# Performance work log

Hardware: AMD Instinct MI355X
Metric: run time of the kernel (lower is better)

Reference implementation:

```python
import jax, jax.numpy as jnp
import numpy as np

N = 50000      # nodes
E = 800000     # edges
F_IN = 128     # input feature dim (OGBN-MAG paper features)
H = 4          # attention heads
HID = 64       # hidden_dim (per-head out channels)
HC = H * HID   # 256, concat output width
NC = 349       # num_classes
BN_EPS = 1e-5


def setup_inputs() -> dict:
    key = jax.random.key(0)
    ks = jax.random.split(key, 32)
    s = 0.05
    inp = {
        "x": jax.random.normal(ks[0], (N, F_IN), dtype=jnp.float32),
        "edge_index": jax.random.randint(ks[1], (2, E), 0, N, dtype=jnp.int64),
    }
    dins = [F_IN, HC]
    i = 2
    for l in range(2):
        d = dins[l]
        inp[f"ws{l}"] = jax.random.normal(ks[i], (d, HC), jnp.float32) * s; i += 1
        inp[f"wd{l}"] = jax.random.normal(ks[i], (d, HC), jnp.float32) * s; i += 1
        inp[f"atts{l}"] = jax.random.normal(ks[i], (H, HID), jnp.float32) * s; i += 1
        inp[f"attd{l}"] = jax.random.normal(ks[i], (H, HID), jnp.float32) * s; i += 1
        inp[f"bg{l}"] = jnp.zeros((HC,), jnp.float32); i += 1
        inp[f"lw{l}"] = jax.random.normal(ks[i], (d, HC), jnp.float32) * s; i += 1
        inp[f"lb{l}"] = jnp.zeros((HC,), jnp.float32); i += 1
        inp[f"g{l}"] = jnp.ones((HC,), jnp.float32); i += 1
        inp[f"b{l}"] = jnp.zeros((HC,), jnp.float32); i += 1
    inp["fcw"] = jax.random.normal(ks[i], (HC, NC), jnp.float32) * s
    inp["fcb"] = jnp.zeros((NC,), jnp.float32)
    return inp


def _gat(x, src, dst, ws, wd, atts, attd, bias):
    # PyG GATConv: separate src/dst projections, per-edge additive attention,
    # softmax over incoming edges of each dst node, scatter-add aggregation.
    n = x.shape[0]
    xs = (x @ ws).reshape(n, H, HID)            # [N,H,C] source messages
    xd = (x @ wd).reshape(n, H, HID)
    a_s = jnp.einsum("nhc,hc->nh", xs, atts)    # alpha_src
    a_d = jnp.einsum("nhc,hc->nh", xd, attd)    # alpha_dst
    e = jax.nn.leaky_relu(a_s[src] + a_d[dst], 0.2)   # [E,H]
    m = jax.ops.segment_max(e, dst, num_segments=n)   # segment-softmax (stable)
    ex = jnp.exp(e - m[dst])
    den = jax.ops.segment_sum(ex, dst, num_segments=n)
    w = ex / (den[dst] + 1e-16)                 # [E,H]
    out = jax.ops.segment_sum(xs[src] * w[:, :, None], dst, num_segments=n)
    return out.reshape(n, HC) + bias


def _bn(h, gamma, beta):
    # training-mode BatchNorm1d: batch statistics over nodes, biased variance
    mu = jnp.mean(h, axis=0)
    var = jnp.mean(jnp.square(h - mu), axis=0)
    return (h - mu) * jax.lax.rsqrt(var + BN_EPS) * gamma + beta


def reference(x, edge_index, ws0, wd0, atts0, attd0, bg0, lw0, lb0, g0, b0,
              ws1, wd1, atts1, attd1, bg1, lw1, lb1, g1, b1, fcw, fcb):
    src, dst = edge_index[0], edge_index[1]
    h = _gat(x, src, dst, ws0, wd0, atts0, attd0, bg0) + x @ lw0 + lb0
    h = jax.nn.relu(_bn(h, g0, b0))
    h = _gat(h, src, dst, ws1, wd1, atts1, attd1, bg1) + h @ lw1 + lb1
    h = jax.nn.relu(_bn(h, g1, b1))
    return h @ fcw + fcb
```

## Files before the change

kernel.cpp:

```cpp
#include <hip/hip_runtime.h>
#include <hip/hip_bf16.h>
#include <math.h>

#define N_NODES 50000
#define MPAD 50048
#define N_EDGES 800000
#define HCH 256
#define NHEAD 4
#define HIDC 64
#define NCLS 349
#define F_IN 128

typedef short short8 __attribute__((ext_vector_type(8)));
typedef float floatx4 __attribute__((ext_vector_type(4)));

__global__ void k_detect(const unsigned* ei, int* flag) {
    if (blockIdx.x == 0 && threadIdx.x == 0) {
        int i64 = 1;
        for (int e = 0; e < 64; e++)
            if (ei[2 * e + 1] != 0u) { i64 = 0; break; }
        *flag = i64;
    }
}

__device__ __forceinline__ void edge_sd(const int* ei, int e, int i64, int& s, int& d) {
    if (i64) {
        const long long* p = (const long long*)ei;
        s = (int)p[e]; d = (int)p[N_EDGES + e];
    } else {
        s = ei[e]; d = ei[N_EDGES + e];
    }
}

__global__ void k_deg(const int* ei, const int* flag, int* deg) {
    int e = blockIdx.x * 256 + threadIdx.x;
    if (e >= N_EDGES) return;
    int s, d; edge_sd(ei, e, *flag, s, d);
    atomicAdd(&deg[d], 1);
}

__global__ __launch_bounds__(256) void k_scan1(const int* __restrict__ deg,
                                               int* __restrict__ rowptr,
                                               int* __restrict__ bsum) {
    __shared__ int sd[256];
    int t = threadIdx.x;
    int base = blockIdx.x * 1024 + t * 4;
    int d0 = 0, d1 = 0, d2 = 0, d3 = 0;
    if (base + 3 < N_NODES) {
        int4 v = *(const int4*)(deg + base);
        d0 = v.x; d1 = v.y; d2 = v.z; d3 = v.w;
    } else {
        if (base + 0 < N_NODES) d0 = deg[base + 0];
        if (base + 1 < N_NODES) d1 = deg[base + 1];
        if (base + 2 < N_NODES) d2 = deg[base + 2];
        if (base + 3 < N_NODES) d3 = deg[base + 3];
    }
    int ts = d0 + d1 + d2 + d3;
    sd[t] = ts;
    __syncthreads();
    #pragma unroll
    for (int off = 1; off < 256; off <<= 1) {
        int v = (t >= off) ? sd[t - off] : 0;
        __syncthreads();
        sd[t] += v;
        __syncthreads();
    }
    int excl = (t == 0) ? 0 : sd[t - 1];
    if (base + 0 < N_NODES) rowptr[base + 0] = excl;
    if (base + 1 < N_NODES) rowptr[base + 1] = excl + d0;
    if (base + 2 < N_NODES) rowptr[base + 2] = excl + d0 + d1;
    if (base + 3 < N_NODES) rowptr[base + 3] = excl + d0 + d1 + d2;
    if (t == 255) bsum[blockIdx.x] = sd[255];
}

__global__ void k_scan2(int* __restrict__ bsum, int nb, int* __restrict__ rowptr) {
    int lane = threadIdx.x;
    int orig = (lane < nb) ? bsum[lane] : 0;
    int v = orig;
    #pragma unroll
    for (int off = 1; off < 64; off <<= 1) {
        int tv = __shfl_up(v, off, 64);
        if (lane >= off) v += tv;
    }
    if (lane < nb) bsum[lane] = v - orig;
    if (lane == 0) rowptr[N_NODES] = N_EDGES;
}

__global__ __launch_bounds__(256) void k_scan3(int* __restrict__ rowptr,
                                               const int* __restrict__ bsum) {
    int base = blockIdx.x * 1024 + threadIdx.x * 4;
    int off = bsum[blockIdx.x];
    if (base + 3 < N_NODES) {
        int4 v = *(int4*)(rowptr + base);
        v.x += off; v.y += off; v.z += off; v.w += off;
        *(int4*)(rowptr + base) = v;
    } else {
        for (int j = 0; j < 4; j++)
            if (base + j < N_NODES) rowptr[base + j] += off;
    }
}

__global__ void k_fill(const int* ei, const int* flag, const int* __restrict__ rowptr,
                       int* cursor, int* __restrict__ esrc) {
    int e = blockIdx.x * 256 + threadIdx.x;
    if (e >= N_EDGES) return;
    int s, d; edge_sd(ei, e, *flag, s, d);
    int pos = atomicAdd(&cursor[d], 1);
    esrc[rowptr[d] + pos] = s;
}

__global__ void k_wtilde(const float* __restrict__ ws, const float* __restrict__ wd,
                         const float* __restrict__ atts, const float* __restrict__ attd,
                         float* __restrict__ wt, int d) {
    int id = blockIdx.x * 256 + threadIdx.x;
    if (id >= d * 8) return;
    int j = id & 7, k = id >> 3;
    const float* w = (j < 4) ? ws : wd;
    const float* at = (j < 4) ? atts : attd;
    int h = j & 3;
    float s = 0.f;
    for (int c = 0; c < HIDC; c++) s += w[k * HCH + h * HIDC + c] * at[h * HIDC + c];
    wt[k * 8 + j] = s;
}

__device__ __forceinline__ unsigned short b16(float v) {
    __hip_bfloat16 t = __float2bfloat16(v);
    return *(unsigned short*)&t;
}

__device__ __forceinline__ float bfu(unsigned short u) {
    unsigned v = (unsigned)u << 16;
    return __builtin_bit_cast(float, v);
}

__global__ __launch_bounds__(256) void k_xcast(const float* __restrict__ x,
                                               unsigned short* __restrict__ xb) {
    size_t tot = (size_t)N_NODES * 128 / 4;
    for (size_t i = (size_t)blockIdx.x * 256 + threadIdx.x; i < tot;
         i += (size_t)gridDim.x * 256) {
        float4 v = *(const float4*)(x + i * 4);
        ushort4 o = {b16(v.x), b16(v.y), b16(v.z), b16(v.w)};
        *(ushort4*)(xb + i * 4) = o;
    }
}

__global__ void k_wcat_t(const float* __restrict__ ws, const float* __restrict__ lw,
                         const float* __restrict__ wtil, int K,
                         unsigned short* __restrict__ Bb) {
    int id = blockIdx.x * 256 + threadIdx.x;
    if (id >= 640 * K) return;
    int c = id / K, k = id % K;
    float v;
    if (c < 256) v = ws[(size_t)k * 256 + c];
    else if (c < 512) v = lw[(size_t)k * 256 + (c - 256)];
    else if (c < 520) v = wtil[(size_t)k * 8 + (c - 512)];
    else v = 0.f;
    Bb[(size_t)c * K + k] = b16(v);
}

__global__ void k_fcw_t(const float* __restrict__ fcw, int K,
                        unsigned short* __restrict__ Bb) {
    int id = blockIdx.x * 256 + threadIdx.x;
    if (id >= 384 * K) return;
    int c = id / K, k = id % K;
    float v = (c < NCLS) ? fcw[(size_t)k * NCLS + c] : 0.f;
    Bb[(size_t)c * K + k] = b16(v);
}

__device__ __forceinline__ void gload16(const void* g, void* l) {
    __builtin_amdgcn_global_load_lds(
        (const __attribute__((address_space(1))) void*)g,
        (__attribute__((address_space(3))) void*)l, 16, 0, 0);
}

__global__ __launch_bounds__(256) void k_gemm1(
    const unsigned short* __restrict__ Ab,
    const unsigned short* __restrict__ Bb,
    float* __restrict__ C, int ldc, __hip_bfloat16* __restrict__ xsb,
    __hip_bfloat16* __restrict__ linbb, float* __restrict__ aout,
    const float* __restrict__ bias, int M, int K, int Nc) {
    __shared__ unsigned short sA[2][4096];
    __shared__ unsigned short sB[2][4096];
    int tid = threadIdx.x;
    int lane = tid & 63, wave = tid >> 6;
    int wm = wave >> 1, wn = wave & 1;
    int row0 = blockIdx.x * 128, col0 = blockIdx.y * 128;

    int rowq[2], kcq[2];
    #pragma unroll
    for (int q = 0; q < 2; q++) {
        int lds16 = wave * 128 + q * 64 + lane;
        int line = lds16 >> 3;
        int slot0 = (lds16 & 7) ^ (line & 7);
        rowq[q] = (line << 1) | (slot0 >> 2);
        kcq[q] = slot0 & 3;
    }
    int kc = lane >> 4, fr = lane & 15;
    int offA[4], offB[4];
    #pragma unroll
    for (int i = 0; i < 4; i++) {
        int ar = wm * 64 + i * 16 + fr;
        int ln = ar >> 1;
        int sl = (((ar & 1) << 2) | kc) ^ (ln & 7);
        offA[i] = ln * 128 + sl * 16;
        int bc = wn * 64 + i * 16 + fr;
        ln = bc >> 1;
        sl = (((bc & 1) << 2) | kc) ^ (ln & 7);
        offB[i] = ln * 128 + sl * 16;
    }

    const int nt = K >> 5;
    #pragma unroll
    for (int q = 0; q < 2; q++) {
        int lb = wave * 2048 + q * 1024;
        gload16(Ab + (size_t)(row0 + rowq[q]) * K + kcq[q] * 8, (char*)sA[0] + lb);
        gload16(Bb + (size_t)(col0 + rowq[q]) * K + kcq[q] * 8, (char*)sB[0] + lb);
    }

    floatx4 acc[4][4] = {};
    int cur = 0;
    for (int t = 0; t < nt; t++) {
        if (t + 1 < nt) {
            int k0 = (t + 1) << 5;
            #pragma unroll
            for (int q = 0; q < 2; q++) {
                int lb = wave * 2048 + q * 1024;
                gload16(Ab + (size_t)(row0 + rowq[q]) * K + k0 + kcq[q] * 8, (char*)sA[cur ^ 1] + lb);
                gload16(Bb + (size_t)(col0 + rowq[q]) * K + k0 + kcq[q] * 8, (char*)sB[cur ^ 1] + lb);
            }
            asm volatile("s_waitcnt vmcnt(4)" ::: "memory");
        } else {
            asm volatile("s_waitcnt vmcnt(0)" ::: "memory");
        }
        __builtin_amdgcn_s_barrier();
        __builtin_amdgcn_sched_barrier(0);
        short8 fah[4], fbh[4];
        #pragma unroll
        for (int i = 0; i < 4; i++) {
            fah[i] = *(const short8*)((const char*)sA[cur] + offA[i]);
            fbh[i] = *(const short8*)((const char*)sB[cur] + offB[i]);
        }
        #pragma unroll
        for (int i = 0; i < 4; i++)
            #pragma unroll
            for (int j = 0; j < 4; j++)
                acc[i][j] = __builtin_amdgcn_mfma_f32_16x16x32_bf16(fah[i], fbh[j], acc[i][j], 0, 0, 0);
        asm volatile("s_waitcnt lgkmcnt(0)" ::: "memory");
        __builtin_amdgcn_s_barrier();
        __builtin_amdgcn_sched_barrier(0);
        cur ^= 1;
    }
    #pragma unroll
    for (int i = 0; i < 4; i++) {
        #pragma unroll
        for (int j = 0; j < 4; j++) {
            int c = col0 + wn * 64 + j * 16 + fr;
            if (c >= Nc) continue;
            float bv = bias ? bias[c] : 0.f;
            #pragma unroll
            for (int q = 0; q < 4; q++) {
                int r = row0 + wm * 64 + i * 16 + (lane >> 4) * 4 + q;
                if (r >= M) continue;
                float val = acc[i][j][q] + bv;
                if (C) C[(size_t)r * ldc + c] = val;
                else if (c < 256) xsb[(size_t)r * 256 + c] = __float2bfloat16(val);
                else if (c < 512) linbb[(size_t)r * 256 + (c - 256)] = __float2bfloat16(val);
                else aout[(size_t)r * 8 + (c - 512)] = val;
            }
        }
    }
}

#define LEAKY_EXP(vv) __expf(((vv) > 0.f) ? (vv) : 0.2f * (vv))

__global__ __launch_bounds__(256) void k_agg(
    const __hip_bfloat16* __restrict__ xsb,
    const __hip_bfloat16* __restrict__ linb, const float* __restrict__ a,
    const int* __restrict__ rowptr, const int* __restrict__ esrc,
    const float* __restrict__ bg, const float* __restrict__ lb,
    __hip_bfloat16* __restrict__ hout) {
    int wave = threadIdx.x >> 6;
    int lane = threadIdx.x & 63;
    int n = blockIdx.x * 4 + wave;
    if (n >= N_NODES) return;
    int half = lane >> 5;
    int l32 = lane & 31;
    int c0 = l32 * 8;
    int h = l32 >> 3;
    float ad = a[(size_t)n * 8 + 4 + h];
    int beg = rowptr[n], end = rowptr[n + 1];
    float acc[8] = {};
    float dsum = 0.f;
    int k = beg;
    for (; k + 8 <= end; k += 8) {
        int sb = k + half * 4;
        int s[4];
        #pragma unroll
        for (int u = 0; u < 4; u++) s[u] = esrc[sb + u];
        short8 m[4];
        #pragma unroll
        for (int u = 0; u < 4; u++)
            m[u] = *(const short8*)(xsb + (size_t)s[u] * 256 + c0);
        float av[4];
        #pragma unroll
        for (int u = 0; u < 4; u++) av[u] = a[(size_t)s[u] * 8 + h];
        #pragma unroll
        for (int u = 0; u < 4; u++) {
            float ev = LEAKY_EXP(av[u] + ad);
            #pragma unroll
            for (int j = 0; j < 8; j++)
                acc[j] += bfu((unsigned short)m[u][j]) * ev;
            dsum += ev;
        }
    }
    for (; k < end; k += 2) {
        int idx = k + half;
        bool valid = idx < end;
        int s = esrc[valid ? idx : (end - 1)];
        short8 m = *(const short8*)(xsb + (size_t)s * 256 + c0);
        float av = a[(size_t)s * 8 + h];
        float ev = valid ? LEAKY_EXP(av + ad) : 0.f;
        #pragma unroll
        for (int j = 0; j < 8; j++)
            acc[j] += bfu((unsigned short)m[j]) * ev;
        dsum += ev;
    }
    #pragma unroll
    for (int j = 0; j < 8; j++) acc[j] += __shfl_xor(acc[j], 32, 64);
    dsum += __shfl_xor(dsum, 32, 64);
    if (lane < 32) {
        float inv = 1.f / (dsum + 1e-16f);
        float4 bg0 = *(const float4*)(bg + c0);
        float4 bg1 = *(const float4*)(bg + c0 + 4);
        float4 lb0 = *(const float4*)(lb + c0);
        float4 lb1 = *(const float4*)(lb + c0 + 4);
        float bgv[8] = {bg0.x, bg0.y, bg0.z, bg0.w, bg1.x, bg1.y, bg1.z, bg1.w};
        float lbv[8] = {lb0.x, lb0.y, lb0.z, lb0.w, lb1.x, lb1.y, lb1.z, lb1.w};
        short8 lnv = *(const short8*)(linb + (size_t)n * 256 + c0);
        short8 o;
        #pragma unroll
        for (int j = 0; j < 8; j++)
            o[j] = (short)b16(acc[j] * inv + bgv[j] + bfu((unsigned short)lnv[j]) + lbv[j]);
        *(short8*)(hout + (size_t)n * 256 + c0) = o;
    }
}

__global__ void k_bnstats(const __hip_bfloat16* __restrict__ hb,
                          float* __restrict__ bnsum, float* __restrict__ bnsq) {
    int c = threadIdx.x;
    float s = 0.f, q = 0.f;
    for (int r = blockIdx.x; r < N_NODES; r += gridDim.x) {
        float v = __bfloat162float(hb[(size_t)r * 256 + c]);
        s += v; q += v * v;
    }
    atomicAdd(&bnsum[c], s);
    atomicAdd(&bnsq[c], q);
}

__global__ __launch_bounds__(256) void k_bnapply(
    const __hip_bfloat16* __restrict__ hb, __hip_bfloat16* __restrict__ hpost,
    const float* __restrict__ bnsum, const float* __restrict__ bnsq,
    const float* __restrict__ g, const float* __restrict__ b) {
    __shared__ float sA[256], sB[256];
    int t = threadIdx.x;
    {
        float m = bnsum[t] / (float)N_NODES;
        float v = bnsq[t] / (float)N_NODES - m * m;
        float rs = rsqrtf(v + 1e-5f) * g[t];
        sA[t] = rs;
        sB[t] = b[t] - m * rs;
    }
    __syncthreads();
    size_t tot = (size_t)N_NODES * 256;
    for (size_t i = (size_t)blockIdx.x * 256 + t; i < tot;
         i += (size_t)gridDim.x * 256) {
        int c = (int)(i & 255);
        float v = __bfloat162float(hb[i]) * sA[c] + sB[c];
        v = v > 0.f ? v : 0.f;
        hpost[i] = __float2bfloat16(v);
    }
}

extern "C" void kernel_launch(void* const* d_in, const int* in_sizes, int n_in,
                              void* d_out, int out_size, void* d_ws, size_t ws_size,
                              hipStream_t stream) {
    const float* x     = (const float*)d_in[0];
    const int*   ei    = (const int*)d_in[1];
    const float* ws0   = (const float*)d_in[2];
    const float* wd0   = (const float*)d_in[3];
    const float* atts0 = (const float*)d_in[4];
    const float* attd0 = (const float*)d_in[5];
    const float* bg0   = (const float*)d_in[6];
    const float* lw0   = (const float*)d_in[7];
    const float* lb0   = (const float*)d_in[8];
    const float* g0    = (const float*)d_in[9];
    const float* b0    = (const float*)d_in[10];
    const float* ws1   = (const float*)d_in[11];
    const float* wd1   = (const float*)d_in[12];
    const float* atts1 = (const float*)d_in[13];
    const float* attd1 = (const float*)d_in[14];
    const float* bg1   = (const float*)d_in[15];
    const float* lw1   = (const float*)d_in[16];
    const float* lb1   = (const float*)d_in[17];
    const float* g1    = (const float*)d_in[18];
    const float* b1    = (const float*)d_in[19];
    const float* fcw   = (const float*)d_in[20];
    const float* fcb   = (const float*)d_in[21];
    float* out = (float*)d_out;

    char* p = (char*)d_ws;
    auto alloc = [&](size_t bytes) -> char* {
        char* r = p;
        p += (bytes + 255) & ~(size_t)255;
        return r;
    };
    __hip_bfloat16* xsb   = (__hip_bfloat16*)alloc((size_t)N_NODES * 256 * 2);
    __hip_bfloat16* linb  = (__hip_bfloat16*)alloc((size_t)N_NODES * 256 * 2);
    __hip_bfloat16* hb    = (__hip_bfloat16*)alloc((size_t)N_NODES * 256 * 2);
    __hip_bfloat16* hpost = (__hip_bfloat16*)alloc((size_t)MPAD * 256 * 2);
    unsigned short* xb    = (unsigned short*)alloc((size_t)MPAD * 128 * 2);
    float* a      = (float*)alloc((size_t)N_NODES * 8 * 4);
    int*   esrc   = (int*)alloc((size_t)N_EDGES * 4);
    int*   rowptr = (int*)alloc((size_t)(N_NODES + 1) * 4);
    int*   bsum   = (int*)alloc(64 * 4);
    unsigned short* w0b = (unsigned short*)alloc((size_t)640 * 128 * 2);
    unsigned short* w1b = (unsigned short*)alloc((size_t)640 * 256 * 2);
    unsigned short* fcb16 = (unsigned short*)alloc((size_t)384 * 256 * 2);
    float* wtil   = (float*)alloc((size_t)256 * 8 * 4);
    int*   flag   = (int*)alloc(256);
    size_t zr_bytes = (size_t)N_NODES * 4 * 2 + 4 * 256 * 4;
    char* zbase = alloc(zr_bytes);
    int*   deg    = (int*)zbase;
    int*   cursor = deg + N_NODES;
    float* bnsum0 = (float*)(cursor + N_NODES);
    float* bnsq0  = bnsum0 + 256;
    float* bnsum1 = bnsq0 + 256;
    float* bnsq1  = bnsum1 + 256;

    hipMemsetAsync(zbase, 0, zr_bytes, stream);

    const int EB = (N_EDGES + 255) / 256;
    const int RB = MPAD / 128;
    const int AB = (N_NODES + 3) / 4;
    const int SB = (N_NODES + 1023) / 1024;

    k_detect<<<1, 1, 0, stream>>>((const unsigned*)ei, flag);
    k_deg<<<EB, 256, 0, stream>>>(ei, flag, deg);
    k_scan1<<<SB, 256, 0, stream>>>(deg, rowptr, bsum);
    k_scan2<<<1, 64, 0, stream>>>(bsum, SB, rowptr);
    k_scan3<<<SB, 256, 0, stream>>>(rowptr, bsum);
    k_fill<<<EB, 256, 0, stream>>>(ei, flag, rowptr, cursor, esrc);

    k_wtilde<<<(128 * 8 + 255) / 256, 256, 0, stream>>>(ws0, wd0, atts0, attd0, wtil, 128);
    k_wcat_t<<<(640 * 128 + 255) / 256, 256, 0, stream>>>(ws0, lw0, wtil, 128, w0b);
    k_wtilde<<<(256 * 8 + 255) / 256, 256, 0, stream>>>(ws1, wd1, atts1, attd1, wtil, 256);
    k_wcat_t<<<(640 * 256 + 255) / 256, 256, 0, stream>>>(ws1, lw1, wtil, 256, w1b);
    k_fcw_t<<<(384 * 256 + 255) / 256, 256, 0, stream>>>(fcw, 256, fcb16);
    k_xcast<<<2048, 256, 0, stream>>>(x, xb);

    k_gemm1<<<dim3(RB, 5), 256, 0, stream>>>(xb, w0b,
                                             nullptr, 0, xsb, linb, a,
                                             nullptr, N_NODES, 128, 520);
    k_agg<<<AB, 256, 0, stream>>>(xsb, linb, a, rowptr, esrc, bg0, lb0, hb);
    k_bnstats<<<1024, 256, 0, stream>>>(hb, bnsum0, bnsq0);
    k_bnapply<<<2048, 256, 0, stream>>>(hb, hpost, bnsum0, bnsq0, g0, b0);

    k_gemm1<<<dim3(RB, 5), 256, 0, stream>>>((const unsigned short*)hpost, w1b,
                                             nullptr, 0, xsb, linb, a,
                                             nullptr, N_NODES, 256, 520);
    k_agg<<<AB, 256, 0, stream>>>(xsb, linb, a, rowptr, esrc, bg1, lb1, hb);
    k_bnstats<<<1024, 256, 0, stream>>>(hb, bnsum1, bnsq1);
    k_bnapply<<<2048, 256, 0, stream>>>(hb, hpost, bnsum1, bnsq1, g1, b1);

    k_gemm1<<<dim3(RB, 3), 256, 0, stream>>>((const unsigned short*)hpost, fcb16,
                                             out, NCLS, nullptr, nullptr, nullptr,
                                             fcb, N_NODES, 256, NCLS);
}
```

Before: 491.8 us.

## Split GAT features into column-group-major layout and aggregate per 32-column slice

The GEMM epilogue now writes the xs and lin projections in a layout blocked into eight 32-column groups, each stored node-major. The aggregation kernel launches eight times as many blocks, each handling one column group, so gathered neighbour rows for a group stay within a 16 MB slice that is more likely to stay cache-resident. The GEMM also skips MFMAs and LDS reads for column tiles past Nc. The cost is that the edge list and attention logits are read eight times, and each lane now handles only two channels with narrower loads.

```diff
diff --git a/kernel.cpp b/kernel.cpp
--- a/kernel.cpp
+++ b/kernel.cpp
@@ -197,6 +197,7 @@
     }
     int kc = lane >> 4, fr = lane & 15;
     int offA[4], offB[4];
+    bool usej[4];
     #pragma unroll
     for (int i = 0; i < 4; i++) {
         int ar = wm * 64 + i * 16 + fr;
@@ -207,6 +208,7 @@
         ln = bc >> 1;
         sl = (((bc & 1) << 2) | kc) ^ (ln & 7);
         offB[i] = ln * 128 + sl * 16;
+        usej[i] = (col0 + wn * 64 + i * 16) < Nc;
     }
 
     const int nt = K >> 5;
@@ -238,13 +240,14 @@
         #pragma unroll
         for (int i = 0; i < 4; i++) {
             fah[i] = *(const short8*)((const char*)sA[cur] + offA[i]);
-            fbh[i] = *(const short8*)((const char*)sB[cur] + offB[i]);
+            if (usej[i]) fbh[i] = *(const short8*)((const char*)sB[cur] + offB[i]);
         }
         #pragma unroll
         for (int i = 0; i < 4; i++)
             #pragma unroll
             for (int j = 0; j < 4; j++)
-                acc[i][j] = __builtin_amdgcn_mfma_f32_16x16x32_bf16(fah[i], fbh[j], acc[i][j], 0, 0, 0);
+                if (usej[j])
+                    acc[i][j] = __builtin_amdgcn_mfma_f32_16x16x32_bf16(fah[i], fbh[j], acc[i][j], 0, 0, 0);
         asm volatile("s_waitcnt lgkmcnt(0)" ::: "memory");
         __builtin_amdgcn_s_barrier();
         __builtin_amdgcn_sched_barrier(0);
@@ -254,6 +257,7 @@
     for (int i = 0; i < 4; i++) {
         #pragma unroll
         for (int j = 0; j < 4; j++) {
+            if (!usej[j]) continue;
             int c = col0 + wn * 64 + j * 16 + fr;
             if (c >= Nc) continue;
             float bv = bias ? bias[c] : 0.f;
@@ -263,9 +267,13 @@
                 if (r >= M) continue;
                 float val = acc[i][j][q] + bv;
                 if (C) C[(size_t)r * ldc + c] = val;
-                else if (c < 256) xsb[(size_t)r * 256 + c] = __float2bfloat16(val);
-                else if (c < 512) linbb[(size_t)r * 256 + (c - 256)] = __float2bfloat16(val);
-                else aout[(size_t)r * 8 + (c - 512)] = val;
+                else if (c < 256)
+                    xsb[((size_t)(c >> 5) * N_NODES + r) * 32 + (c & 31)] = __float2bfloat16(val);
+                else if (c < 512) {
+                    int c2 = c - 256;
+                    linbb[((size_t)(c2 >> 5) * N_NODES + r) * 32 + (c2 & 31)] = __float2bfloat16(val);
+                } else
+                    aout[(size_t)r * 8 + (c - 512)] = val;
             }
         }
     }
@@ -274,74 +282,62 @@
 #define LEAKY_EXP(vv) __expf(((vv) > 0.f) ? (vv) : 0.2f * (vv))
 
 __global__ __launch_bounds__(256) void k_agg(
-    const __hip_bfloat16* __restrict__ xsb,
-    const __hip_bfloat16* __restrict__ linb, const float* __restrict__ a,
+    const __hip_bfloat16* __restrict__ xsb2,
+    const __hip_bfloat16* __restrict__ linb2,
+    const float* __restrict__ a,
     const int* __restrict__ rowptr, const int* __restrict__ esrc,
     const float* __restrict__ bg, const float* __restrict__ lb,
     __hip_bfloat16* __restrict__ hout) {
+    int g = blockIdx.x & 7;
+    int nb = blockIdx.x >> 3;
     int wave = threadIdx.x >> 6;
     int lane = threadIdx.x & 63;
-    int n = blockIdx.x * 4 + wave;
+    int n = nb * 4 + wave;
     if (n >= N_NODES) return;
-    int half = lane >> 5;
-    int l32 = lane & 31;
-    int c0 = l32 * 8;
-    int h = l32 >> 3;
+    int slot = lane >> 4, l16 = lane & 15;
+    int cg = g * 32 + l16 * 2;
+    int h = g >> 1;
+    const __hip_bfloat16* xg = xsb2 + (size_t)g * N_NODES * 32;
     float ad = a[(size_t)n * 8 + 4 + h];
     int beg = rowptr[n], end = rowptr[n + 1];
-    float acc[8] = {};
-    float dsum = 0.f;
+    float a0 = 0.f, a1 = 0.f, dsum = 0.f;
     int k = beg;
     for (; k + 8 <= end; k += 8) {
-        int sb = k + half * 4;
-        int s[4];
-        #pragma unroll
-        for (int u = 0; u < 4; u++) s[u] = esrc[sb + u];
-        short8 m[4];
-        #pragma unroll
-        for (int u = 0; u < 4; u++)
-            m[u] = *(const short8*)(xsb + (size_t)s[u] * 256 + c0);
-        float av[4];
-        #pragma unroll
-        for (int u = 0; u < 4; u++) av[u] = a[(size_t)s[u] * 8 + h];
-        #pragma unroll
-        for (int u = 0; u < 4; u++) {
-            float ev = LEAKY_EXP(av[u] + ad);
-            #pragma unroll
-            for (int j = 0; j < 8; j++)
-                acc[j] += bfu((unsigned short)m[u][j]) * ev;
-            dsum += ev;
-        }
-    }
-    for (; k < end; k += 2) {
-        int idx = k + half;
+        int s0 = esrc[k + slot];
+        int s1 = esrc[k + 4 + slot];
+        ushort2 m0 = *(const ushort2*)(xg + (size_t)s0 * 32 + l16 * 2);
+        ushort2 m1 = *(const ushort2*)(xg + (size_t)s1 * 32 + l16 * 2);
+        float av0 = a[(size_t)s0 * 8 + h];
+        float av1 = a[(size_t)s1 * 8 + h];
+        float e0 = LEAKY_EXP(av0 + ad);
+        float e1 = LEAKY_EXP(av1 + ad);
+        a0 += bfu(m0.x) * e0 + bfu(m1.x) * e1;
+        a1 += bfu(m0.y) * e0 + bfu(m1.y) * e1;
+        dsum += e0 + e1;
+    }
+    for (; k < end; k += 4) {
+        int idx = k + slot;
         bool valid = idx < end;
         int s = esrc[valid ? idx : (end - 1)];
-        short8 m = *(const short8*)(xsb + (size_t)s * 256 + c0);
+        ushort2 m = *(const ushort2*)(xg + (size_t)s * 32 + l16 * 2);
         float av = a[(size_t)s * 8 + h];
         float ev = valid ? LEAKY_EXP(av + ad) : 0.f;
-        #pragma unroll
-        for (int j = 0; j < 8; j++)
-            acc[j] += bfu((unsigned short)m[j]) * ev;
+        a0 += bfu(m.x) * ev;
+        a1 += bfu(m.y) * ev;
         dsum += ev;
     }
-    #pragma unroll
-    for (int j = 0; j < 8; j++) acc[j] += __shfl_xor(acc[j], 32, 64);
-    dsum += __shfl_xor(dsum, 32, 64);
-    if (lane < 32) {
+    a0 += __shfl_xor(a0, 16, 64); a0 += __shfl_xor(a0, 32, 64);
+    a1 += __shfl_xor(a1, 16, 64); a1 += __shfl_xor(a1, 32, 64);
+    dsum += __shfl_xor(dsum, 16, 64); dsum += __shfl_xor(dsum, 32, 64);
+    if (slot == 0) {
         float inv = 1.f / (dsum + 1e-16f);
-        float4 bg0 = *(const float4*)(bg + c0);
-        float4 bg1 = *(const float4*)(bg + c0 + 4);
-        float4 lb0 = *(const float4*)(lb + c0);
-        float4 lb1 = *(const float4*)(lb + c0 + 4);
-        float bgv[8] = {bg0.x, bg0.y, bg0.z, bg0.w, bg1.x, bg1.y, bg1.z, bg1.w};
-        float lbv[8] = {lb0.x, lb0.y, lb0.z, lb0.w, lb1.x, lb1.y, lb1.z, lb1.w};
-        short8 lnv = *(const short8*)(linb + (size_t)n * 256 + c0);
-        short8 o;
-        #pragma unroll
-        for (int j = 0; j < 8; j++)
-            o[j] = (short)b16(acc[j] * inv + bgv[j] + bfu((unsigned short)lnv[j]) + lbv[j]);
-        *(short8*)(hout + (size_t)n * 256 + c0) = o;
+        float2 bgv = *(const float2*)(bg + cg);
+        float2 lbv = *(const float2*)(lb + cg);
+        ushort2 lnv = *(const ushort2*)(linb2 + ((size_t)g * N_NODES + n) * 32 + l16 * 2);
+        ushort2 o;
+        o.x = b16(a0 * inv + bgv.x + bfu(lnv.x) + lbv.x);
+        o.y = b16(a1 * inv + bgv.y + bfu(lnv.y) + lbv.y);
+        *(ushort2*)(hout + (size_t)n * 256 + cg) = o;
     }
 }
 
@@ -441,7 +437,7 @@
 
     const int EB = (N_EDGES + 255) / 256;
     const int RB = MPAD / 128;
-    const int AB = (N_NODES + 3) / 4;
+    const int AB = 8 * ((N_NODES + 3) / 4);
     const int SB = (N_NODES + 1023) / 1024;
 
     k_detect<<<1, 1, 0, stream>>>((const unsigned*)ei, flag);
```

Result: slower. 760.3 us (+54.6%).
